# Performance work log

Measured on AMD Instinct MI355X. Metric: run time of the kernel, lower is better.

The kernel has to match this reference:

```python
import jax, jax.numpy as jnp
import numpy as np

TOPK = 2  # config.topk_exp


def setup_inputs() -> dict:
    key = jax.random.key(0)
    ks = jax.random.split(key, 4)
    B, S, D, F, E = 4, 1024, 768, 3072, 8
    scale_in = 1.0 / np.sqrt(D)
    scale_hid = 1.0 / np.sqrt(F)
    return {
        "x": jax.random.normal(ks[0], (B, S, D), dtype=jnp.float32),
        "router_w": jax.random.normal(ks[1], (E, D), dtype=jnp.float32) * scale_in,
        "w_fc": jax.random.normal(ks[2], (E, D, F), dtype=jnp.float32) * scale_in,
        "b_fc": jnp.zeros((E, F), dtype=jnp.float32),
        "w_proj": jax.random.normal(ks[3], (E, F, D), dtype=jnp.float32) * scale_hid,
        "b_proj": jnp.zeros((E, D), dtype=jnp.float32),
    }


def _moe_forward(x, router_w, w_fc, b_fc, w_proj, b_proj):
    B, S, D = x.shape
    E = router_w.shape[0]
    xt = x.reshape(-1, D)  # [T, D] tokens
    # per-token router: Linear(D, E, bias=False)
    gate_logits = xt @ router_w.T  # [T, E]
    # topk_exp > 1: raw logits -> topk -> softmax over the k selected logits
    weights, selected = jax.lax.top_k(gate_logits, TOPK)  # [T, k]
    weights = jax.nn.softmax(weights.astype(jnp.float32), axis=1).astype(x.dtype)
    # combine weights per expert: w[t, e] = sum_k weights[t,k] * (selected[t,k]==e)
    onehot = jax.nn.one_hot(selected, E, dtype=x.dtype)  # [T, k, E]
    comb = jnp.einsum('tk,tke->te', weights, onehot)  # [T, E]
    # expert MLP (GPT-2 style: fc -> gelu -> proj), evaluated densely then combined
    h = jax.nn.gelu(jnp.einsum('td,edf->etf', xt, w_fc) + b_fc[:, None, :], approximate=False)
    y = jnp.einsum('etf,efd->etd', h, w_proj) + b_proj[:, None, :]  # [E, T, D]
    out = jnp.einsum('te,etd->td', comb, y)  # weighted scatter-combine
    return out.reshape(B, S, D)


def reference(x, router_w, w_fc, b_fc, w_proj, b_proj):
    return _moe_forward(x, router_w, w_fc, b_fc, w_proj, b_proj)
```

## Files before the change

kernel.cpp:

```cpp
#include <hip/hip_runtime.h>
#include <hip/hip_bf16.h>

#define TT 4096
#define DD 768
#define FF 3072
#define EE 8
#define NSLOT 8192
#define NSLOT_PAD 8320

#define WAITCNT_VM4 0x0F74
#define WAITCNT_VM7 0x0F77

typedef __attribute__((ext_vector_type(8))) short bf16x8;
typedef __attribute__((ext_vector_type(4))) float f32x4;
typedef const __attribute__((address_space(1))) void* gas1_t;
typedef __attribute__((address_space(3))) void* las3_t;

__global__ __launch_bounds__(256) void router2_kernel(const float* __restrict__ x,
    const float* __restrict__ rw, int* __restrict__ tokE, float* __restrict__ tokW,
    int* __restrict__ blkCnt) {
  __shared__ float rws[EE * 832];
  __shared__ int cnt_s[EE];
  int tid = threadIdx.x;
  if (tid < EE) cnt_s[tid] = 0;
#pragma unroll
  for (int k = 0; k < 6; ++k) {
    int c = tid + k * 256;
    int e = c / 192, rem = c % 192;
    int s = rem / 12, i = rem % 12;
    float4 v = *(const float4*)&rw[e * DD + s * 48 + i * 4];
    *(float4*)&rws[e * 832 + s * 52 + i * 4] = v;
  }
  __syncthreads();
  int lane = tid & 63;
  int sl = lane & 15;
  int t = blockIdx.x * 16 + (tid >> 6) * 4 + (lane >> 4);
  const float4* xp = (const float4*)(x + (size_t)t * DD + sl * 48);
  float acc[EE];
#pragma unroll
  for (int e = 0; e < EE; ++e) acc[e] = 0.f;
#pragma unroll
  for (int i = 0; i < 12; ++i) {
    float4 xv = xp[i];
#pragma unroll
    for (int e = 0; e < EE; ++e) {
      float4 rv = *(const float4*)&rws[e * 832 + sl * 52 + i * 4];
      acc[e] = fmaf(xv.x, rv.x, fmaf(xv.y, rv.y, fmaf(xv.z, rv.z, fmaf(xv.w, rv.w, acc[e]))));
    }
  }
#pragma unroll
  for (int off = 8; off > 0; off >>= 1) {
#pragma unroll
    for (int e = 0; e < EE; ++e) acc[e] += __shfl_xor(acc[e], off);
  }
  if (sl == 0) {
    float v0 = -1e30f; int e0 = 0;
#pragma unroll
    for (int e = 0; e < EE; ++e) { if (acc[e] > v0) { v0 = acc[e]; e0 = e; } }
    float v1 = -1e30f; int e1 = 0;
#pragma unroll
    for (int e = 0; e < EE; ++e) { if (e != e0 && acc[e] > v1) { v1 = acc[e]; e1 = e; } }
    float w1 = 1.f / (1.f + __expf(v0 - v1));
    float w0 = 1.f - w1;
    tokE[2 * t] = e0; tokE[2 * t + 1] = e1;
    tokW[2 * t] = w0; tokW[2 * t + 1] = w1;
    atomicAdd(&cnt_s[e0], 1);
    atomicAdd(&cnt_s[e1], 1);
  }
  __syncthreads();
  if (tid < EE) blkCnt[blockIdx.x * EE + tid] = cnt_s[tid];
}

__global__ __launch_bounds__(256) void offsets2_kernel(const int* __restrict__ blkCnt,
    int* __restrict__ offs, int* __restrict__ blkBase,
    int* __restrict__ tile1, int* __restrict__ tile2, int* __restrict__ meta) {
  __shared__ int wsum[4][EE];
  int tid = threadIdx.x;
  int lane = tid & 63, w = tid >> 6;
  int c[EE], s[EE];
#pragma unroll
  for (int e = 0; e < EE; ++e) { c[e] = blkCnt[tid * EE + e]; s[e] = c[e]; }
#pragma unroll
  for (int off = 1; off < 64; off <<= 1) {
#pragma unroll
    for (int e = 0; e < EE; ++e) {
      int v = __shfl_up(s[e], off);
      if (lane >= off) s[e] += v;
    }
  }
  if (lane == 63) {
#pragma unroll
    for (int e = 0; e < EE; ++e) wsum[w][e] = s[e];
  }
  __syncthreads();
#pragma unroll
  for (int e = 0; e < EE; ++e) {
    int pre = 0;
    for (int w2 = 0; w2 < w; ++w2) pre += wsum[w2][e];
    s[e] += pre;
  }
  int tot[EE];
#pragma unroll
  for (int e = 0; e < EE; ++e) tot[e] = wsum[0][e] + wsum[1][e] + wsum[2][e] + wsum[3][e];
  int offl[EE + 1];
  offl[0] = 0;
#pragma unroll
  for (int e = 0; e < EE; ++e) offl[e + 1] = offl[e] + tot[e];
#pragma unroll
  for (int e = 0; e < EE; ++e) blkBase[tid * EE + e] = offl[e] + s[e] - c[e];
  if (tid == 0) {
    for (int e = 0; e <= EE; ++e) offs[e] = offl[e];
    int n1 = 0, n2 = 0;
    for (int e = 0; e < EE; ++e) { n1 += (tot[e] + 127) / 128; n2 += (tot[e] + 63) / 64; }
    meta[0] = n1; meta[1] = n2;
  }
  if (tid < EE) {
    int p1 = 0, p2 = 0;
    for (int e = 0; e < tid; ++e) { p1 += (tot[e] + 127) / 128; p2 += (tot[e] + 63) / 64; }
    for (int m = 0; m < tot[tid]; m += 128) tile1[p1++] = (tid << 20) | m;
    for (int m = 0; m < tot[tid]; m += 64)  tile2[p2++] = (tid << 20) | m;
  }
}

__global__ __launch_bounds__(256) void scatter_gather2_kernel(const float* __restrict__ x,
    const int* __restrict__ tokE, const float* __restrict__ tokW,
    const int* __restrict__ blkBase, int* __restrict__ slotIdx, float* __restrict__ slotW,
    int* __restrict__ slotTok, __hip_bfloat16* __restrict__ Xg) {
  __shared__ int base_s[EE], lcur[EE];
  __shared__ int sl_s[16][2];
  int tid = threadIdx.x;
  int b = blockIdx.x;
  if (tid < EE) { base_s[tid] = blkBase[b * EE + tid]; lcur[tid] = 0; }
  __syncthreads();
  if (tid < 16) {
    int t = b * 16 + tid;
    int e0 = tokE[2 * t], e1 = tokE[2 * t + 1];
    int s0 = base_s[e0] + atomicAdd(&lcur[e0], 1);
    int s1 = base_s[e1] + atomicAdd(&lcur[e1], 1);
    slotIdx[2 * t] = s0; slotIdx[2 * t + 1] = s1;
    slotW[s0] = tokW[2 * t]; slotW[s1] = tokW[2 * t + 1];
    slotTok[s0] = t; slotTok[s1] = t;
    sl_s[tid][0] = s0; sl_s[tid][1] = s1;
  }
  __syncthreads();
  int k = tid >> 4, p = tid & 15;
  int t = b * 16 + k;
  int s0 = sl_s[k][0], s1 = sl_s[k][1];
  const float4* src = (const float4*)(x + (size_t)t * DD);
  ushort4* d0 = (ushort4*)(Xg + (size_t)s0 * DD);
  ushort4* d1 = (ushort4*)(Xg + (size_t)s1 * DD);
#pragma unroll
  for (int i = 0; i < 12; ++i) {
    int idx = i * 16 + p;
    float4 v = src[idx];
    union { ushort4 u; __hip_bfloat16 h[4]; } cv;
    cv.h[0] = __float2bfloat16(v.x);
    cv.h[1] = __float2bfloat16(v.y);
    cv.h[2] = __float2bfloat16(v.z);
    cv.h[3] = __float2bfloat16(v.w);
    d0[idx] = cv.u;
    d1[idx] = cv.u;
  }
}

__global__ void transpose_convert_kernel(const float* __restrict__ w_fc, __hip_bfloat16* __restrict__ wfcT,
                                         const float* __restrict__ w_proj, __hip_bfloat16* __restrict__ wprojT) {
  __shared__ float tile[64][65];
  int bx = blockIdx.x;
  const float* S; __hip_bfloat16* D; int K, N, n0, k0;
  if (bx < 576) { S = w_fc;   D = wfcT;   K = DD; N = FF; n0 = (bx % 48) * 64; k0 = (bx / 48) * 64; }
  else { bx -= 576; S = w_proj; D = wprojT; K = FF; N = DD; n0 = (bx % 12) * 64; k0 = (bx / 12) * 64; }
  S += (size_t)blockIdx.z * K * N;
  D += (size_t)blockIdx.z * K * N;
  int tid = threadIdx.x;
#pragma unroll
  for (int i = 0; i < 4; ++i) {
    int slot = i * 256 + tid;
    int r = slot >> 4, c4 = slot & 15;
    float4 v = *(const float4*)&S[(size_t)(k0 + r) * N + n0 + c4 * 4];
    tile[r][c4 * 4 + 0] = v.x; tile[r][c4 * 4 + 1] = v.y;
    tile[r][c4 * 4 + 2] = v.z; tile[r][c4 * 4 + 3] = v.w;
  }
  __syncthreads();
#pragma unroll
  for (int i = 0; i < 4; ++i) {
    int slot = i * 256 + tid;
    int n = slot >> 4, kc = slot & 15;
    union { ushort4 u; __hip_bfloat16 h[4]; } cv;
    cv.h[0] = __float2bfloat16(tile[kc * 4 + 0][n]);
    cv.h[1] = __float2bfloat16(tile[kc * 4 + 1][n]);
    cv.h[2] = __float2bfloat16(tile[kc * 4 + 2][n]);
    cv.h[3] = __float2bfloat16(tile[kc * 4 + 3][n]);
    *(ushort4*)&D[(size_t)(n0 + n) * K + k0 + kc * 4] = cv.u;
  }
}

__device__ __forceinline__ float gelu_f(float v) {
  float z = v * 0.70710678118654752f;
  float az = fabsf(z);
  float t = 1.0f / (1.0f + 0.3275911f * az);
  float poly = t * (0.254829592f + t * (-0.284496736f + t * (1.421413741f +
               t * (-1.453152027f + t * 1.061405429f))));
  float erf_abs = 1.0f - poly * __expf(-az * az);
  float erf = copysignf(erf_abs, z);
  return 0.5f * v * (1.0f + erf);
}

__device__ __forceinline__ int swz4(int m) { return (m + (m >> 2)) & 3; }

__global__ __launch_bounds__(256) void gemm1_kernel(const __hip_bfloat16* __restrict__ Xg,
    const __hip_bfloat16* __restrict__ wfcT, const float* __restrict__ b_fc,
    __hip_bfloat16* __restrict__ H, const int* __restrict__ offs,
    const int* __restrict__ tile1, const int* __restrict__ meta) {
  __shared__ __align__(16) short As[2][128 * 32];
  __shared__ __align__(16) short Bs[2][128 * 32];
  if ((int)blockIdx.y >= meta[0]) return;
  int tv = tile1[blockIdx.y];
  int e = tv >> 20;
  int m_base = tv & 0xFFFFF;
  int off_e = offs[e];
  int n_e = offs[e + 1] - off_e;
  int n0 = blockIdx.x * 128;
  const short* A = (const short*)Xg + (size_t)(off_e + m_base) * DD;
  const short* B = (const short*)wfcT + (size_t)e * FF * DD + (size_t)n0 * DD;
  int tid = threadIdx.x;
  int lane = tid & 63, wid = tid >> 6;
  int l15 = lane & 15, q = lane >> 4;
  int wm = wid & 1, wn = wid >> 1;
  int fs0 = tid, fs1 = tid + 256;
  int m0 = fs0 >> 2, c0 = (fs0 & 3) ^ swz4(m0);
  int m1 = fs1 >> 2, c1 = (fs1 & 3) ^ swz4(m1);
  const short* gA0 = A + (size_t)m0 * DD + c0 * 8;
  const short* gA1 = A + (size_t)m1 * DD + c1 * 8;
  const short* gB0 = B + (size_t)m0 * DD + c0 * 8;
  const short* gB1 = B + (size_t)m1 * DD + c1 * 8;
  int aoff[4], boff[4];
#pragma unroll
  for (int mi = 0; mi < 4; ++mi) {
    int r = wm * 64 + mi * 16 + l15;
    aoff[mi] = (r * 4 + (q ^ swz4(r))) * 8;
  }
#pragma unroll
  for (int ni = 0; ni < 4; ++ni) {
    int r = wn * 64 + ni * 16 + l15;
    boff[ni] = (r * 4 + (q ^ swz4(r))) * 8;
  }
  f32x4 acc[4][4] = {};
  __builtin_amdgcn_global_load_lds((gas1_t)gA0, (las3_t)(&As[0][0] + fs0 * 8), 16, 0, 0);
  __builtin_amdgcn_global_load_lds((gas1_t)gA1, (las3_t)(&As[0][0] + fs1 * 8), 16, 0, 0);
  __builtin_amdgcn_global_load_lds((gas1_t)gB0, (las3_t)(&Bs[0][0] + fs0 * 8), 16, 0, 0);
  __builtin_amdgcn_global_load_lds((gas1_t)gB1, (las3_t)(&Bs[0][0] + fs1 * 8), 16, 0, 0);
  gA0 += 32; gA1 += 32; gB0 += 32; gB1 += 32;
  for (int it = 0; it < DD / 32; ++it) {
    int cur = it & 1, nxt = cur ^ 1;
    short* curA = &As[cur][0];
    short* curB = &Bs[cur][0];
    __builtin_amdgcn_s_barrier();
    __builtin_amdgcn_global_load_lds((gas1_t)gA0, (las3_t)(&As[nxt][0] + fs0 * 8), 16, 0, 0);
    __builtin_amdgcn_global_load_lds((gas1_t)gA1, (las3_t)(&As[nxt][0] + fs1 * 8), 16, 0, 0);
    __builtin_amdgcn_global_load_lds((gas1_t)gB0, (las3_t)(&Bs[nxt][0] + fs0 * 8), 16, 0, 0);
    __builtin_amdgcn_global_load_lds((gas1_t)gB1, (las3_t)(&Bs[nxt][0] + fs1 * 8), 16, 0, 0);
    gA0 += 32; gA1 += 32; gB0 += 32; gB1 += 32;
    __builtin_amdgcn_s_waitcnt(WAITCNT_VM4);
    __builtin_amdgcn_s_barrier();
    bf16x8 af[4], bfr[4];
#pragma unroll
    for (int mi = 0; mi < 4; ++mi) af[mi] = *(const bf16x8*)(curA + aoff[mi]);
#pragma unroll
    for (int ni = 0; ni < 4; ++ni) bfr[ni] = *(const bf16x8*)(curB + boff[ni]);
#pragma unroll
    for (int mi = 0; mi < 4; ++mi)
#pragma unroll
      for (int ni = 0; ni < 4; ++ni)
        acc[mi][ni] = __builtin_amdgcn_mfma_f32_16x16x32_bf16(af[mi], bfr[ni], acc[mi][ni], 0, 0, 0);
  }
  float bias[4];
#pragma unroll
  for (int ni = 0; ni < 4; ++ni) bias[ni] = b_fc[e * FF + n0 + wn * 64 + ni * 16 + l15];
  __hip_bfloat16* Hp = H + (size_t)(off_e + m_base) * FF + n0;
#pragma unroll
  for (int mi = 0; mi < 4; ++mi) {
#pragma unroll
    for (int r = 0; r < 4; ++r) {
      int ml = wm * 64 + mi * 16 + q * 4 + r;
      if (m_base + ml < n_e) {
#pragma unroll
        for (int ni = 0; ni < 4; ++ni) {
          int nl = wn * 64 + ni * 16 + l15;
          float v = acc[mi][ni][r] + bias[ni];
          Hp[(size_t)ml * FF + nl] = __float2bfloat16(gelu_f(v));
        }
      }
    }
  }
}

__global__ __launch_bounds__(256) void gemm2_kernel(const __hip_bfloat16* __restrict__ H,
    const __hip_bfloat16* __restrict__ wprojT, const float* __restrict__ b_proj,
    const float* __restrict__ slotW, const int* __restrict__ slotTok,
    float* __restrict__ out, const int* __restrict__ offs,
    const int* __restrict__ tile2, const int* __restrict__ meta) {
  __shared__ __align__(16) short As[2][64 * 32];
  __shared__ __align__(16) short Bs[2][384 * 32];
  if ((int)blockIdx.y >= meta[1]) return;
  int tv = tile2[blockIdx.y];
  int e = tv >> 20;
  int m_base = tv & 0xFFFFF;
  int off_e = offs[e];
  int n_e = offs[e + 1] - off_e;
  int n0 = blockIdx.x * 384;
  const short* A = (const short*)H + (size_t)(off_e + m_base) * FF;
  const short* B = (const short*)wprojT + (size_t)e * DD * FF + (size_t)n0 * FF;
  int tid = threadIdx.x;
  int lane = tid & 63, wid = tid >> 6;
  int l15 = lane & 15, q = lane >> 4;
  int mA = tid >> 2, cA = (tid & 3) ^ swz4(mA);
  const short* gA = A + (size_t)mA * FF + cA * 8;
  const short* gB[6];
  int fsB[6];
#pragma unroll
  for (int i = 0; i < 6; ++i) {
    int fs = tid + i * 256;
    int m = fs >> 2, c = (fs & 3) ^ swz4(m);
    fsB[i] = fs;
    gB[i] = B + (size_t)m * FF + c * 8;
  }
  int aoff[4], boff[6];
#pragma unroll
  for (int mi = 0; mi < 4; ++mi) {
    int r = mi * 16 + l15;
    aoff[mi] = (r * 4 + (q ^ swz4(r))) * 8;
  }
#pragma unroll
  for (int ni = 0; ni < 6; ++ni) {
    int r = wid * 96 + ni * 16 + l15;
    boff[ni] = (r * 4 + (q ^ swz4(r))) * 8;
  }
  f32x4 acc[4][6] = {};
  __builtin_amdgcn_global_load_lds((gas1_t)gA, (las3_t)(&As[0][0] + tid * 8), 16, 0, 0);
#pragma unroll
  for (int i = 0; i < 6; ++i)
    __builtin_amdgcn_global_load_lds((gas1_t)gB[i], (las3_t)(&Bs[0][0] + fsB[i] * 8), 16, 0, 0);
  gA += 32;
#pragma unroll
  for (int i = 0; i < 6; ++i) gB[i] += 32;
  for (int it = 0; it < FF / 32; ++it) {
    int cur = it & 1, nxt = cur ^ 1;
    short* curA = &As[cur][0];
    short* curB = &Bs[cur][0];
    __builtin_amdgcn_s_barrier();
    __builtin_amdgcn_global_load_lds((gas1_t)gA, (las3_t)(&As[nxt][0] + tid * 8), 16, 0, 0);
#pragma unroll
    for (int i = 0; i < 6; ++i)
      __builtin_amdgcn_global_load_lds((gas1_t)gB[i], (las3_t)(&Bs[nxt][0] + fsB[i] * 8), 16, 0, 0);
    gA += 32;
#pragma unroll
    for (int i = 0; i < 6; ++i) gB[i] += 32;
    __builtin_amdgcn_s_waitcnt(WAITCNT_VM7);
    __builtin_amdgcn_s_barrier();
    bf16x8 af[4], bfr[6];
#pragma unroll
    for (int mi = 0; mi < 4; ++mi) af[mi] = *(const bf16x8*)(curA + aoff[mi]);
#pragma unroll
    for (int ni = 0; ni < 6; ++ni) bfr[ni] = *(const bf16x8*)(curB + boff[ni]);
#pragma unroll
    for (int mi = 0; mi < 4; ++mi)
#pragma unroll
      for (int ni = 0; ni < 6; ++ni)
        acc[mi][ni] = __builtin_amdgcn_mfma_f32_16x16x32_bf16(af[mi], bfr[ni], acc[mi][ni], 0, 0, 0);
  }
  float bias[6];
#pragma unroll
  for (int ni = 0; ni < 6; ++ni) bias[ni] = b_proj[e * DD + n0 + wid * 96 + ni * 16 + l15];
#pragma unroll
  for (int mi = 0; mi < 4; ++mi) {
#pragma unroll
    for (int r = 0; r < 4; ++r) {
      int ml = mi * 16 + q * 4 + r;
      if (m_base + ml < n_e) {
        int slot = off_e + m_base + ml;
        float w = slotW[slot];
        int tok = slotTok[slot];
        float* op = out + (size_t)tok * DD + n0 + wid * 96;
#pragma unroll
        for (int ni = 0; ni < 6; ++ni)
          atomicAdd(&op[ni * 16 + l15], w * (acc[mi][ni][r] + bias[ni]));
      }
    }
  }
}

extern "C" void kernel_launch(void* const* d_in, const int* in_sizes, int n_in,
                              void* d_out, int out_size, void* d_ws, size_t ws_size,
                              hipStream_t stream) {
  const float* x        = (const float*)d_in[0];
  const float* router_w = (const float*)d_in[1];
  const float* w_fc     = (const float*)d_in[2];
  const float* b_fc     = (const float*)d_in[3];
  const float* w_proj   = (const float*)d_in[4];
  const float* b_proj   = (const float*)d_in[5];
  float* out = (float*)d_out;

  char* p = (char*)d_ws;
  auto alloc = [&](size_t bytes) {
    char* r = p;
    p += (bytes + 255) & ~(size_t)255;
    return r;
  };
  __hip_bfloat16* wfcT   = (__hip_bfloat16*)alloc((size_t)EE * FF * DD * 2);
  __hip_bfloat16* wprojT = (__hip_bfloat16*)alloc((size_t)EE * DD * FF * 2);
  __hip_bfloat16* Xg     = (__hip_bfloat16*)alloc((size_t)NSLOT_PAD * DD * 2);
  __hip_bfloat16* H      = (__hip_bfloat16*)alloc((size_t)NSLOT_PAD * FF * 2);
  int*   tokE    = (int*)alloc(TT * 2 * 4);
  float* tokW    = (float*)alloc(TT * 2 * 4);
  int*   slotIdx = (int*)alloc(TT * 2 * 4);
  float* slotW   = (float*)alloc(NSLOT_PAD * 4);
  int*   slotTok = (int*)alloc(NSLOT_PAD * 4);
  int*   blkCnt  = (int*)alloc(256 * EE * 4);
  int*   blkBase = (int*)alloc(256 * EE * 4);
  int*   tile1   = (int*)alloc(128 * 4);
  int*   tile2   = (int*)alloc(256 * 4);
  int*   offs    = (int*)alloc(64);
  int*   meta    = (int*)alloc(64);

  hipMemsetAsync(out, 0, (size_t)out_size * 4, stream);
  router2_kernel<<<256, 256, 0, stream>>>(x, router_w, tokE, tokW, blkCnt);
  offsets2_kernel<<<1, 256, 0, stream>>>(blkCnt, offs, blkBase, tile1, tile2, meta);
  scatter_gather2_kernel<<<256, 256, 0, stream>>>(x, tokE, tokW, blkBase, slotIdx, slotW, slotTok, Xg);
  transpose_convert_kernel<<<dim3(1152, 1, EE), 256, 0, stream>>>(w_fc, wfcT, w_proj, wprojT);
  gemm1_kernel<<<dim3(FF / 128, 72), 256, 0, stream>>>(Xg, wfcT, b_fc, H, offs, tile1, meta);
  gemm2_kernel<<<dim3(DD / 384, 136), 256, 0, stream>>>(H, wprojT, b_proj, slotW, slotTok, out, offs, tile2, meta);
}
```

Measured before the change: 396.8 us.

## Retile gemm2 to 128x128 blocks with split-K over two halves

The second expert GEMM moves from 64x384 tiles over the tile2 list to 128x128 tiles over the tile1 list, and splits the K dimension (F) into two halves along grid z. The halves are accumulated through the existing atomicAdd combine, with the bias added only by the first half. This is meant to raise block count and occupancy for the small-M per-expert GEMM. In exchange it doubles the atomic traffic to the output and the number of output-epilogue passes.

```diff
diff --git a/kernel.cpp b/kernel.cpp
--- a/kernel.cpp
+++ b/kernel.cpp
@@ -299,91 +299,86 @@
     const __hip_bfloat16* __restrict__ wprojT, const float* __restrict__ b_proj,
     const float* __restrict__ slotW, const int* __restrict__ slotTok,
     float* __restrict__ out, const int* __restrict__ offs,
-    const int* __restrict__ tile2, const int* __restrict__ meta) {
-  __shared__ __align__(16) short As[2][64 * 32];
-  __shared__ __align__(16) short Bs[2][384 * 32];
-  if ((int)blockIdx.y >= meta[1]) return;
-  int tv = tile2[blockIdx.y];
+    const int* __restrict__ tile1, const int* __restrict__ meta) {
+  __shared__ __align__(16) short As[2][128 * 32];
+  __shared__ __align__(16) short Bs[2][128 * 32];
+  if ((int)blockIdx.y >= meta[0]) return;
+  int tv = tile1[blockIdx.y];
   int e = tv >> 20;
   int m_base = tv & 0xFFFFF;
   int off_e = offs[e];
   int n_e = offs[e + 1] - off_e;
-  int n0 = blockIdx.x * 384;
-  const short* A = (const short*)H + (size_t)(off_e + m_base) * FF;
-  const short* B = (const short*)wprojT + (size_t)e * DD * FF + (size_t)n0 * FF;
+  int n0 = blockIdx.x * 128;
+  int kz = blockIdx.z;
+  const short* A = (const short*)H + (size_t)(off_e + m_base) * FF + kz * (FF / 2);
+  const short* B = (const short*)wprojT + (size_t)e * DD * FF + (size_t)n0 * FF + kz * (FF / 2);
   int tid = threadIdx.x;
   int lane = tid & 63, wid = tid >> 6;
   int l15 = lane & 15, q = lane >> 4;
-  int mA = tid >> 2, cA = (tid & 3) ^ swz4(mA);
-  const short* gA = A + (size_t)mA * FF + cA * 8;
-  const short* gB[6];
-  int fsB[6];
-#pragma unroll
-  for (int i = 0; i < 6; ++i) {
-    int fs = tid + i * 256;
-    int m = fs >> 2, c = (fs & 3) ^ swz4(m);
-    fsB[i] = fs;
-    gB[i] = B + (size_t)m * FF + c * 8;
-  }
-  int aoff[4], boff[6];
+  int wm = wid & 1, wn = wid >> 1;
+  int fs0 = tid, fs1 = tid + 256;
+  int m0 = fs0 >> 2, c0 = (fs0 & 3) ^ swz4(m0);
+  int m1 = fs1 >> 2, c1 = (fs1 & 3) ^ swz4(m1);
+  const short* gA0 = A + (size_t)m0 * FF + c0 * 8;
+  const short* gA1 = A + (size_t)m1 * FF + c1 * 8;
+  const short* gB0 = B + (size_t)m0 * FF + c0 * 8;
+  const short* gB1 = B + (size_t)m1 * FF + c1 * 8;
+  int aoff[4], boff[4];
 #pragma unroll
   for (int mi = 0; mi < 4; ++mi) {
-    int r = mi * 16 + l15;
+    int r = wm * 64 + mi * 16 + l15;
     aoff[mi] = (r * 4 + (q ^ swz4(r))) * 8;
   }
 #pragma unroll
-  for (int ni = 0; ni < 6; ++ni) {
-    int r = wid * 96 + ni * 16 + l15;
+  for (int ni = 0; ni < 4; ++ni) {
+    int r = wn * 64 + ni * 16 + l15;
     boff[ni] = (r * 4 + (q ^ swz4(r))) * 8;
   }
-  f32x4 acc[4][6] = {};
-  __builtin_amdgcn_global_load_lds((gas1_t)gA, (las3_t)(&As[0][0] + tid * 8), 16, 0, 0);
-#pragma unroll
-  for (int i = 0; i < 6; ++i)
-    __builtin_amdgcn_global_load_lds((gas1_t)gB[i], (las3_t)(&Bs[0][0] + fsB[i] * 8), 16, 0, 0);
-  gA += 32;
-#pragma unroll
-  for (int i = 0; i < 6; ++i) gB[i] += 32;
-  for (int it = 0; it < FF / 32; ++it) {
+  f32x4 acc[4][4] = {};
+  __builtin_amdgcn_global_load_lds((gas1_t)gA0, (las3_t)(&As[0][0] + fs0 * 8), 16, 0, 0);
+  __builtin_amdgcn_global_load_lds((gas1_t)gA1, (las3_t)(&As[0][0] + fs1 * 8), 16, 0, 0);
+  __builtin_amdgcn_global_load_lds((gas1_t)gB0, (las3_t)(&Bs[0][0] + fs0 * 8), 16, 0, 0);
+  __builtin_amdgcn_global_load_lds((gas1_t)gB1, (las3_t)(&Bs[0][0] + fs1 * 8), 16, 0, 0);
+  gA0 += 32; gA1 += 32; gB0 += 32; gB1 += 32;
+  for (int it = 0; it < FF / 64; ++it) {
     int cur = it & 1, nxt = cur ^ 1;
     short* curA = &As[cur][0];
     short* curB = &Bs[cur][0];
     __builtin_amdgcn_s_barrier();
-    __builtin_amdgcn_global_load_lds((gas1_t)gA, (las3_t)(&As[nxt][0] + tid * 8), 16, 0, 0);
-#pragma unroll
-    for (int i = 0; i < 6; ++i)
-      __builtin_amdgcn_global_load_lds((gas1_t)gB[i], (las3_t)(&Bs[nxt][0] + fsB[i] * 8), 16, 0, 0);
-    gA += 32;
-#pragma unroll
-    for (int i = 0; i < 6; ++i) gB[i] += 32;
-    __builtin_amdgcn_s_waitcnt(WAITCNT_VM7);
+    __builtin_amdgcn_global_load_lds((gas1_t)gA0, (las3_t)(&As[nxt][0] + fs0 * 8), 16, 0, 0);
+    __builtin_amdgcn_global_load_lds((gas1_t)gA1, (las3_t)(&As[nxt][0] + fs1 * 8), 16, 0, 0);
+    __builtin_amdgcn_global_load_lds((gas1_t)gB0, (las3_t)(&Bs[nxt][0] + fs0 * 8), 16, 0, 0);
+    __builtin_amdgcn_global_load_lds((gas1_t)gB1, (las3_t)(&Bs[nxt][0] + fs1 * 8), 16, 0, 0);
+    gA0 += 32; gA1 += 32; gB0 += 32; gB1 += 32;
+    __builtin_amdgcn_s_waitcnt(WAITCNT_VM4);
     __builtin_amdgcn_s_barrier();
-    bf16x8 af[4], bfr[6];
+    bf16x8 af[4], bfr[4];
 #pragma unroll
     for (int mi = 0; mi < 4; ++mi) af[mi] = *(const bf16x8*)(curA + aoff[mi]);
 #pragma unroll
-    for (int ni = 0; ni < 6; ++ni) bfr[ni] = *(const bf16x8*)(curB + boff[ni]);
+    for (int ni = 0; ni < 4; ++ni) bfr[ni] = *(const bf16x8*)(curB + boff[ni]);
 #pragma unroll
     for (int mi = 0; mi < 4; ++mi)
 #pragma unroll
-      for (int ni = 0; ni < 6; ++ni)
+      for (int ni = 0; ni < 4; ++ni)
         acc[mi][ni] = __builtin_amdgcn_mfma_f32_16x16x32_bf16(af[mi], bfr[ni], acc[mi][ni], 0, 0, 0);
   }
-  float bias[6];
-#pragma unroll
-  for (int ni = 0; ni < 6; ++ni) bias[ni] = b_proj[e * DD + n0 + wid * 96 + ni * 16 + l15];
+  float bias[4];
+#pragma unroll
+  for (int ni = 0; ni < 4; ++ni)
+    bias[ni] = (kz == 0) ? b_proj[e * DD + n0 + wn * 64 + ni * 16 + l15] : 0.f;
 #pragma unroll
   for (int mi = 0; mi < 4; ++mi) {
 #pragma unroll
     for (int r = 0; r < 4; ++r) {
-      int ml = mi * 16 + q * 4 + r;
+      int ml = wm * 64 + mi * 16 + q * 4 + r;
       if (m_base + ml < n_e) {
         int slot = off_e + m_base + ml;
         float w = slotW[slot];
         int tok = slotTok[slot];
-        float* op = out + (size_t)tok * DD + n0 + wid * 96;
-#pragma unroll
-        for (int ni = 0; ni < 6; ++ni)
+        float* op = out + (size_t)tok * DD + n0 + wn * 64;
+#pragma unroll
+        for (int ni = 0; ni < 4; ++ni)
           atomicAdd(&op[ni * 16 + l15], w * (acc[mi][ni][r] + bias[ni]));
       }
     }
@@ -429,5 +424,5 @@
   scatter_gather2_kernel<<<256, 256, 0, stream>>>(x, tokE, tokW, blkBase, slotIdx, slotW, slotTok, Xg);
   transpose_convert_kernel<<<dim3(1152, 1, EE), 256, 0, stream>>>(w_fc, wfcT, w_proj, wprojT);
   gemm1_kernel<<<dim3(FF / 128, 72), 256, 0, stream>>>(Xg, wfcT, b_fc, H, offs, tile1, meta);
-  gemm2_kernel<<<dim3(DD / 384, 136), 256, 0, stream>>>(H, wprojT, b_proj, slotW, slotTok, out, offs, tile2, meta);
-}
+  gemm2_kernel<<<dim3(DD / 128, 72, 2), 256, 0, stream>>>(H, wprojT, b_proj, slotW, slotTok, out, offs, tile1, meta);
+}
```

New measurement: 417.3 us. 5.2% more time.
